# Kernel optimization log

Measured on AMD Instinct MI355X. Metric: run time of the kernel, lower is better.

The kernel has to match this reference:

```python
import jax, jax.numpy as jnp
import numpy as np

YOLO_INPUT_SIZE = 416.0
SCORE_THRESHOLD = 0.5
IOU_THRESHOLD = 0.45
AREA_THRESHOLD = 0.0005
MAX_OUTPUT_BOXES = 10
NEG = -1e9


def setup_inputs() -> dict:
    key = jax.random.key(0)
    y = jax.random.uniform(key, (64, 10647, 85), dtype=jnp.float32)
    # first 4 channels are xywh in input-pixel units (YOLO decode divides by 416)
    y = y.at[..., 0:2].multiply(YOLO_INPUT_SIZE)          # centers in [0, 416)
    y = y.at[..., 2:4].multiply(YOLO_INPUT_SIZE * 0.3)    # w,h up to ~125 px
    return {"y_pred": y}


def _decode(y_pred):
    flat = y_pred.reshape(-1, y_pred.shape[-1])           # [N, 85]
    box, conf, probs = flat[:, :4], flat[:, 4], flat[:, 5:]
    scores = conf * jnp.max(probs, axis=-1)               # [N]
    classes = jnp.argmax(probs, axis=-1).astype(jnp.int32)
    b = jnp.clip(box / YOLO_INPUT_SIZE, 0.0, 1.0)
    x, y, w, h = b[:, 0], b[:, 1], b[:, 2], b[:, 3]
    x1 = jnp.clip(x - w * 0.5, 0.0, 1.0)
    y1 = jnp.clip(y - h * 0.5, 0.0, 1.0)
    x2 = jnp.clip(x + w * 0.5, 0.0, 1.0)
    y2 = jnp.clip(y + h * 0.5, 0.0, 1.0)
    big_enough = (x2 - x1) * (y2 - y1) > AREA_THRESHOLD
    keep = big_enough & (scores > SCORE_THRESHOLD)
    boxes = jnp.stack([x1, y1, x2, y2], axis=-1)          # [N, 4]
    work = jnp.where(keep, scores, NEG)                   # masked working scores
    return boxes, scores, classes, work


def _iou_one_vs_all(ref, boxes):
    ix1 = jnp.maximum(ref[0], boxes[:, 0])
    iy1 = jnp.maximum(ref[1], boxes[:, 1])
    ix2 = jnp.minimum(ref[2], boxes[:, 2])
    iy2 = jnp.minimum(ref[3], boxes[:, 3])
    inter = jnp.maximum(ix2 - ix1, 0.0) * jnp.maximum(iy2 - iy1, 0.0)
    a_ref = (ref[2] - ref[0]) * (ref[3] - ref[1])
    a_all = (boxes[:, 2] - boxes[:, 0]) * (boxes[:, 3] - boxes[:, 1])
    return inter / (a_ref + a_all - inter + 1e-10)


def _greedy_nms(boxes, work):
    def step(w, _):
        j = jnp.argmax(w)
        v = w[j] > SCORE_THRESHOLD
        iou = _iou_one_vs_all(boxes[j], boxes)
        w = jnp.where(v & (iou > IOU_THRESHOLD), NEG, w)
        w = w.at[j].set(NEG)
        return w, (j.astype(jnp.int32), v)
    _, (idxs, valid) = jax.lax.scan(step, work, None, length=MAX_OUTPUT_BOXES)
    return idxs, valid


def reference(y_pred):
    boxes, scores, classes, work = _decode(y_pred)
    idxs, valid = _greedy_nms(boxes, work)
    # fixed-size (padded) outputs instead of dynamic boolean gather; `valid`
    # marks real detections (original returns only the valid rows)
    sel_boxes = boxes[idxs]                # [10, 4]
    sel_scores = scores[idxs][:, None]     # [10, 1]
    sel_classes = classes[idxs][:, None]   # [10, 1]
    return sel_boxes, sel_scores, sel_classes, valid
```

## Files before the change

kernel.cpp:

```cpp
#include <hip/hip_runtime.h>

#define ROWS   681408
#define NBINS  8192
#define CAP    64
#define TOPK   192
#define SELCAP 256

#define WS_ROW0     4
#define WS_CNT      16
#define WS_BUCKET   8448

__device__ __forceinline__ float clip01(float v) {
    return fminf(fmaxf(v, 0.0f), 1.0f);
}

__global__ void init_kernel(unsigned int* __restrict__ ws) {
    int i = blockIdx.x * 256 + threadIdx.x;
    if (i < NBINS) ws[WS_CNT + i] = 0u;
}

__global__ __launch_bounds__(256) void decode_kernel(
    const float* __restrict__ y, unsigned int* __restrict__ ws)
{
    const int row = blockIdx.x * 256 + threadIdx.x;
    if (row >= ROWS) return;

    const float*  p  = y + (size_t)row * 85;
    const float4* p4 = (const float4*)p;

    float4 f0 = p4[0];
    float4 f1 = p4[1];
    const float cf = f1.x;

    float bv = f1.y; int bc = 0;
    if (f1.z > bv) { bv = f1.z; bc = 1; }
    if (f1.w > bv) { bv = f1.w; bc = 2; }
    #pragma unroll
    for (int j = 2; j <= 20; j++) {
        float4 f = p4[j];
        const int b0 = 4 * j - 5;
        if (f.x > bv) { bv = f.x; bc = b0; }
        if (f.y > bv) { bv = f.y; bc = b0 + 1; }
        if (f.z > bv) { bv = f.z; bc = b0 + 2; }
        if (f.w > bv) { bv = f.w; bc = b0 + 3; }
    }
    {
        float e84 = p[84];
        if (e84 > bv) { bv = e84; bc = 79; }
    }

    const float score = cf * bv;
    float x  = clip01(f0.x / 416.0f);
    float yy = clip01(f0.y / 416.0f);
    float w  = clip01(f0.z / 416.0f);
    float h  = clip01(f0.w / 416.0f);
    float x1 = clip01(x  - w * 0.5f);
    float y1 = clip01(yy - h * 0.5f);
    float x2 = clip01(x  + w * 0.5f);
    float y2 = clip01(yy + h * 0.5f);
    bool keep = (((x2 - x1) * (y2 - y1)) > 0.0005f) && (score > 0.5f);
    if (keep) {
        int bin = (int)((score - 0.5f) * (2.0f * (float)NBINS));
        bin = min(max(bin, 0), NBINS - 1);
        unsigned int pos = atomicAdd(&ws[WS_CNT + bin], 1u);
        if (pos < (unsigned int)CAP) {
            uint2* bucket = (uint2*)&ws[WS_BUCKET];
            bucket[bin * CAP + pos] =
                make_uint2(__float_as_uint(score), (unsigned int)row);
        }
    }
    if (row == 0) {
        float* r0 = (float*)&ws[WS_ROW0];
        r0[0] = score; r0[1] = (float)bc;
        r0[2] = x1; r0[3] = y1; r0[4] = x2; r0[5] = y2;
    }
}

__global__ __launch_bounds__(256) void nms_kernel(
    const float* __restrict__ y, unsigned int* __restrict__ ws,
    float* __restrict__ out)
{
    __shared__ unsigned int chunk[256];
    __shared__ unsigned int fine[32];
    __shared__ unsigned long long keys[SELCAP];
    __shared__ float4 sboxes[SELCAP];
    __shared__ int s_coarse;
    __shared__ int s_bstar;
    __shared__ unsigned int s_m;
    __shared__ int s_picks;
    __shared__ unsigned int s_idx[10];
    __shared__ float s_score[10];
    __shared__ float4 s_box[10];
    __shared__ int s_cls[10];

    const int t = threadIdx.x;
    const uint2* bucket = (const uint2*)&ws[WS_BUCKET];

    unsigned int ssum = 0;
    {
        const uint4* cnt4 = (const uint4*)&ws[WS_CNT];
        #pragma unroll
        for (int i = 0; i < 8; i++) {
            uint4 v = cnt4[t * 8 + i];
            ssum += min(v.x, (unsigned int)CAP) + min(v.y, (unsigned int)CAP)
                  + min(v.z, (unsigned int)CAP) + min(v.w, (unsigned int)CAP);
        }
    }
    chunk[t] = ssum;
    for (int i = t; i < SELCAP; i += 256) keys[i] = 0ull;
    if (t == 0) s_m = 0u;
    __syncthreads();

    for (int off = 1; off < 256; off <<= 1) {
        unsigned int v = chunk[t];
        unsigned int a = (t + off < 256) ? chunk[t + off] : 0u;
        __syncthreads();
        chunk[t] = v + a;
        __syncthreads();
    }
    const unsigned int total  = chunk[0];
    const unsigned int target = (total < (unsigned int)TOPK) ? total
                                                             : (unsigned int)TOPK;

    if (target > 0) {
        if (chunk[t] >= target && (t == 255 || chunk[t + 1] < target))
            s_coarse = t;
        __syncthreads();

        const int cb = s_coarse * 32;
        if (t < 32) fine[t] = min(ws[WS_CNT + cb + t], (unsigned int)CAP);
        __syncthreads();
        for (int off = 1; off < 32; off <<= 1) {
            unsigned int v = 0, a = 0;
            if (t < 32) { v = fine[t]; a = (t + off < 32) ? fine[t + off] : 0u; }
            __syncthreads();
            if (t < 32) fine[t] = v + a;
            __syncthreads();
        }
        const unsigned int base = (s_coarse < 255) ? chunk[s_coarse + 1] : 0u;
        if (t < 32) {
            unsigned int sfx = base + fine[t];
            unsigned int nxt = (t == 31) ? base : base + fine[t + 1];
            if (sfx >= target && nxt < target) s_bstar = cb + t;
        }
    } else {
        if (t == 0) s_bstar = NBINS;
    }
    __syncthreads();

    for (int bin = s_bstar + t; bin < NBINS; bin += 256) {
        unsigned int c = ws[WS_CNT + bin];
        if (c > (unsigned int)CAP) c = CAP;
        for (unsigned int j = 0; j < c; j++) {
            uint2 cv = bucket[bin * CAP + j];
            unsigned int pos = atomicAdd(&s_m, 1u);
            if (pos < (unsigned int)SELCAP)
                keys[pos] = ((unsigned long long)cv.x << 32) |
                            (unsigned long long)(0xFFFFFFFFu - cv.y);
        }
    }
    __syncthreads();
    unsigned int M = s_m;
    if (M > (unsigned int)SELCAP) M = SELCAP;

    for (int k = 2; k <= SELCAP; k <<= 1) {
        for (int j = k >> 1; j > 0; j >>= 1) {
            for (int i = t; i < SELCAP; i += 256) {
                int ixj = i ^ j;
                if (ixj > i) {
                    unsigned long long a = keys[i], b = keys[ixj];
                    bool descSeg = ((i & k) == 0);
                    if (descSeg ? (a < b) : (a > b)) { keys[i] = b; keys[ixj] = a; }
                }
            }
            __syncthreads();
        }
    }

    for (int i = t; i < (int)M; i += 256) {
        unsigned int idx = 0xFFFFFFFFu - (unsigned int)(keys[i] & 0xFFFFFFFFull);
        const float* p = y + (size_t)idx * 85;
        float x  = clip01(p[0] / 416.0f);
        float yy = clip01(p[1] / 416.0f);
        float w  = clip01(p[2] / 416.0f);
        float h  = clip01(p[3] / 416.0f);
        sboxes[i] = make_float4(clip01(x - w * 0.5f), clip01(yy - h * 0.5f),
                                clip01(x + w * 0.5f), clip01(yy + h * 0.5f));
    }
    __syncthreads();

    if (t == 0) {
        int np = 0;
        for (int i = 0; i < (int)M && np < 10; i++) {
            float4 b = sboxes[i];
            bool ok = true;
            for (int kk = 0; kk < np; kk++) {
                float4 r = s_box[kk];
                float ix1 = fmaxf(r.x, b.x);
                float iy1 = fmaxf(r.y, b.y);
                float ix2 = fminf(r.z, b.z);
                float iy2 = fminf(r.w, b.w);
                float inter = fmaxf(ix2 - ix1, 0.0f) * fmaxf(iy2 - iy1, 0.0f);
                float aref = (r.z - r.x) * (r.w - r.y);
                float aall = (b.z - b.x) * (b.w - b.y);
                float iou = inter / (aref + aall - inter + 1e-10f);
                if (iou > 0.45f) { ok = false; break; }
            }
            if (ok) {
                s_box[np] = b;
                s_idx[np] = 0xFFFFFFFFu - (unsigned int)(keys[i] & 0xFFFFFFFFull);
                s_score[np] = __uint_as_float((unsigned int)(keys[i] >> 32));
                np++;
            }
        }
        s_picks = np;
    }
    __syncthreads();

    {
        int p = t >> 4, s = t & 15;
        float bv = -1.0f; int bc = 1 << 20;
        if (p < s_picks) {
            const float* pr = y + (size_t)s_idx[p] * 85 + 5;
            #pragma unroll
            for (int kk = 0; kk < 5; kk++) {
                float v = pr[s + 16 * kk];
                int c = s + 16 * kk;
                if (v > bv) { bv = v; bc = c; }
            }
        }
        #pragma unroll
        for (int m = 8; m >= 1; m >>= 1) {
            float ov = __shfl_xor(bv, m, 64);
            int   oc = __shfl_xor(bc, m, 64);
            if (ov > bv || (ov == bv && oc < bc)) { bv = ov; bc = oc; }
        }
        if (p < s_picks && s == 0) s_cls[p] = bc;
    }
    __syncthreads();

    if (t == 0) {
        const float* r0 = (const float*)&ws[WS_ROW0];
        float score0 = r0[0], class0 = r0[1];
        float4 box0 = make_float4(r0[2], r0[3], r0[4], r0[5]);
        for (int kk = 0; kk < 10; kk++) {
            bool v = kk < s_picks;
            float4 b = v ? s_box[kk] : box0;
            out[4 * kk + 0] = b.x;
            out[4 * kk + 1] = b.y;
            out[4 * kk + 2] = b.z;
            out[4 * kk + 3] = b.w;
            out[40 + kk] = v ? s_score[kk] : score0;
            out[50 + kk] = v ? (float)s_cls[kk] : class0;
            out[60 + kk] = v ? 1.0f : 0.0f;
        }
    }
}

extern "C" void kernel_launch(void* const* d_in, const int* in_sizes, int n_in,
                              void* d_out, int out_size, void* d_ws, size_t ws_size,
                              hipStream_t stream)
{
    const float* y = (const float*)d_in[0];
    unsigned int* ws = (unsigned int*)d_ws;

    init_kernel<<<dim3(NBINS / 256), dim3(256), 0, stream>>>(ws);
    decode_kernel<<<dim3((ROWS + 255) / 256), dim3(256), 0, stream>>>(y, ws);
    nms_kernel<<<dim3(1), dim3(256), 0, stream>>>(y, ws, (float*)d_out);
}
```

Baseline: 85.07 us.

## Split each row across four lanes with coalesced nontemporal loads and shuffle-reduce argmax

```diff
diff --git a/kernel.cpp b/kernel.cpp
--- a/kernel.cpp
+++ b/kernel.cpp
@@ -5,74 +5,180 @@
 #define CAP    64
 #define TOPK   192
 #define SELCAP 256
+#define RPB    128
+#define NBLK   ((ROWS + RPB - 1) / RPB)
 
 #define WS_ROW0     4
 #define WS_CNT      16
 #define WS_BUCKET   8448
 
+typedef float floatx4 __attribute__((ext_vector_type(4)));
+
 __device__ __forceinline__ float clip01(float v) {
     return fminf(fmaxf(v, 0.0f), 1.0f);
 }
 
-__global__ void init_kernel(unsigned int* __restrict__ ws) {
-    int i = blockIdx.x * 256 + threadIdx.x;
-    if (i < NBINS) ws[WS_CNT + i] = 0u;
+__device__ __forceinline__ float4 ntload4(const float4* p) {
+    floatx4 v = __builtin_nontemporal_load((const floatx4*)p);
+    return make_float4(v.x, v.y, v.z, v.w);
 }
 
 __global__ __launch_bounds__(256) void decode_kernel(
     const float* __restrict__ y, unsigned int* __restrict__ ws)
 {
-    const int row = blockIdx.x * 256 + threadIdx.x;
-    if (row >= ROWS) return;
-
-    const float*  p  = y + (size_t)row * 85;
-    const float4* p4 = (const float4*)p;
-
-    float4 f0 = p4[0];
-    float4 f1 = p4[1];
-    const float cf = f1.x;
-
-    float bv = f1.y; int bc = 0;
-    if (f1.z > bv) { bv = f1.z; bc = 1; }
-    if (f1.w > bv) { bv = f1.w; bc = 2; }
+    const int t    = threadIdx.x;
+    const int lane = t & 63;
+    const int wv   = t >> 6;
+    const int s    = lane & 3;
+    const int qr   = lane >> 2;
+    const unsigned int r0 = blockIdx.x * RPB + wv * 32 + qr * 2;
+    if (r0 >= (unsigned int)ROWS) return;
+    const unsigned int r1 = r0 + 1;
+
+    const float*  pA = y + (size_t)r0 * 85;
+    const float*  pB = pA + 85;
+    const float4* a4 = (const float4*)pA;
+    const float4* b4 = (const float4*)pB;
+
+    float4 A0 = ntload4(a4 + s);
+    float4 A1 = ntload4(a4 + s + 4);
+    float4 A2 = ntload4(a4 + s + 8);
+    float4 A3 = ntload4(a4 + s + 12);
+    float4 A4 = ntload4(a4 + s + 16);
+    float4 B0 = ntload4(b4 + s);
+    float4 B1 = ntload4(b4 + s + 4);
+    float4 B2 = ntload4(b4 + s + 8);
+    float4 B3 = ntload4(b4 + s + 12);
+    float4 B4 = ntload4(b4 + s + 16);
+    float4 At = make_float4(-1.0f, -1.0f, -1.0f, -1.0f);
+    float4 Bt = At;
+    float a84 = -1.0f, b84 = -1.0f;
+    if (s == 0) { At = ntload4(a4 + 20); Bt = ntload4(b4 + 20); }
+    if (s == 1) { a84 = pA[84]; b84 = pB[84]; }
+
+    const int b0 = 4 * s;
+    float bvA = -1.0f; int bcA = 1 << 20;
+    {
+        if (b0 + 0 >= 5 && A0.x > bvA) { bvA = A0.x; bcA = b0 - 5; }
+        if (b0 + 1 >= 5 && A0.y > bvA) { bvA = A0.y; bcA = b0 - 4; }
+        if (b0 + 2 >= 5 && A0.z > bvA) { bvA = A0.z; bcA = b0 - 3; }
+        if (b0 + 3 >= 5 && A0.w > bvA) { bvA = A0.w; bcA = b0 - 2; }
+        if (A1.x > bvA) { bvA = A1.x; bcA = b0 + 11; }
+        if (A1.y > bvA) { bvA = A1.y; bcA = b0 + 12; }
+        if (A1.z > bvA) { bvA = A1.z; bcA = b0 + 13; }
+        if (A1.w > bvA) { bvA = A1.w; bcA = b0 + 14; }
+        if (A2.x > bvA) { bvA = A2.x; bcA = b0 + 27; }
+        if (A2.y > bvA) { bvA = A2.y; bcA = b0 + 28; }
+        if (A2.z > bvA) { bvA = A2.z; bcA = b0 + 29; }
+        if (A2.w > bvA) { bvA = A2.w; bcA = b0 + 30; }
+        if (A3.x > bvA) { bvA = A3.x; bcA = b0 + 43; }
+        if (A3.y > bvA) { bvA = A3.y; bcA = b0 + 44; }
+        if (A3.z > bvA) { bvA = A3.z; bcA = b0 + 45; }
+        if (A3.w > bvA) { bvA = A3.w; bcA = b0 + 46; }
+        if (A4.x > bvA) { bvA = A4.x; bcA = b0 + 59; }
+        if (A4.y > bvA) { bvA = A4.y; bcA = b0 + 60; }
+        if (A4.z > bvA) { bvA = A4.z; bcA = b0 + 61; }
+        if (A4.w > bvA) { bvA = A4.w; bcA = b0 + 62; }
+        if (s == 0) {
+            if (At.x > bvA) { bvA = At.x; bcA = 75; }
+            if (At.y > bvA) { bvA = At.y; bcA = 76; }
+            if (At.z > bvA) { bvA = At.z; bcA = 77; }
+            if (At.w > bvA) { bvA = At.w; bcA = 78; }
+        }
+        if (s == 1 && a84 > bvA) { bvA = a84; bcA = 79; }
+    }
+    float bvB = -1.0f; int bcB = 1 << 20;
+    {
+        if (b0 + 0 >= 5 && B0.x > bvB) { bvB = B0.x; bcB = b0 - 5; }
+        if (b0 + 1 >= 5 && B0.y > bvB) { bvB = B0.y; bcB = b0 - 4; }
+        if (b0 + 2 >= 5 && B0.z > bvB) { bvB = B0.z; bcB = b0 - 3; }
+        if (b0 + 3 >= 5 && B0.w > bvB) { bvB = B0.w; bcB = b0 - 2; }
+        if (B1.x > bvB) { bvB = B1.x; bcB = b0 + 11; }
+        if (B1.y > bvB) { bvB = B1.y; bcB = b0 + 12; }
+        if (B1.z > bvB) { bvB = B1.z; bcB = b0 + 13; }
+        if (B1.w > bvB) { bvB = B1.w; bcB = b0 + 14; }
+        if (B2.x > bvB) { bvB = B2.x; bcB = b0 + 27; }
+        if (B2.y > bvB) { bvB = B2.y; bcB = b0 + 28; }
+        if (B2.z > bvB) { bvB = B2.z; bcB = b0 + 29; }
+        if (B2.w > bvB) { bvB = B2.w; bcB = b0 + 30; }
+        if (B3.x > bvB) { bvB = B3.x; bcB = b0 + 43; }
+        if (B3.y > bvB) { bvB = B3.y; bcB = b0 + 44; }
+        if (B3.z > bvB) { bvB = B3.z; bcB = b0 + 45; }
+        if (B3.w > bvB) { bvB = B3.w; bcB = b0 + 46; }
+        if (B4.x > bvB) { bvB = B4.x; bcB = b0 + 59; }
+        if (B4.y > bvB) { bvB = B4.y; bcB = b0 + 60; }
+        if (B4.z > bvB) { bvB = B4.z; bcB = b0 + 61; }
+        if (B4.w > bvB) { bvB = B4.w; bcB = b0 + 62; }
+        if (s == 0) {
+            if (Bt.x > bvB) { bvB = Bt.x; bcB = 75; }
+            if (Bt.y > bvB) { bvB = Bt.y; bcB = 76; }
+            if (Bt.z > bvB) { bvB = Bt.z; bcB = 77; }
+            if (Bt.w > bvB) { bvB = Bt.w; bcB = 78; }
+        }
+        if (s == 1 && b84 > bvB) { bvB = b84; bcB = 79; }
+    }
+
     #pragma unroll
-    for (int j = 2; j <= 20; j++) {
-        float4 f = p4[j];
-        const int b0 = 4 * j - 5;
-        if (f.x > bv) { bv = f.x; bc = b0; }
-        if (f.y > bv) { bv = f.y; bc = b0 + 1; }
-        if (f.z > bv) { bv = f.z; bc = b0 + 2; }
-        if (f.w > bv) { bv = f.w; bc = b0 + 3; }
-    }
-    {
-        float e84 = p[84];
-        if (e84 > bv) { bv = e84; bc = 79; }
-    }
-
-    const float score = cf * bv;
-    float x  = clip01(f0.x / 416.0f);
-    float yy = clip01(f0.y / 416.0f);
-    float w  = clip01(f0.z / 416.0f);
-    float h  = clip01(f0.w / 416.0f);
-    float x1 = clip01(x  - w * 0.5f);
-    float y1 = clip01(yy - h * 0.5f);
-    float x2 = clip01(x  + w * 0.5f);
-    float y2 = clip01(yy + h * 0.5f);
-    bool keep = (((x2 - x1) * (y2 - y1)) > 0.0005f) && (score > 0.5f);
-    if (keep) {
-        int bin = (int)((score - 0.5f) * (2.0f * (float)NBINS));
-        bin = min(max(bin, 0), NBINS - 1);
-        unsigned int pos = atomicAdd(&ws[WS_CNT + bin], 1u);
-        if (pos < (unsigned int)CAP) {
-            uint2* bucket = (uint2*)&ws[WS_BUCKET];
-            bucket[bin * CAP + pos] =
-                make_uint2(__float_as_uint(score), (unsigned int)row);
-        }
-    }
-    if (row == 0) {
-        float* r0 = (float*)&ws[WS_ROW0];
-        r0[0] = score; r0[1] = (float)bc;
-        r0[2] = x1; r0[3] = y1; r0[4] = x2; r0[5] = y2;
+    for (int m = 1; m <= 2; m <<= 1) {
+        float ov = __shfl_xor(bvA, m, 64);
+        int   oc = __shfl_xor(bcA, m, 64);
+        if (ov > bvA || (ov == bvA && oc < bcA)) { bvA = ov; bcA = oc; }
+        float ow = __shfl_xor(bvB, m, 64);
+        int   od = __shfl_xor(bcB, m, 64);
+        if (ow > bvB || (ow == bvB && od < bcB)) { bvB = ow; bcB = od; }
+    }
+
+    const int ql = (lane & 60) + 1;
+    float cfA = __shfl(A0.x, ql, 64);
+    float cfB = __shfl(B0.x, ql, 64);
+
+    if (s == 0) {
+        uint2* bucket = (uint2*)&ws[WS_BUCKET];
+        {
+            float score = cfA * bvA;
+            float x  = clip01(A0.x / 416.0f);
+            float yy = clip01(A0.y / 416.0f);
+            float w  = clip01(A0.z / 416.0f);
+            float h  = clip01(A0.w / 416.0f);
+            float x1 = clip01(x  - w * 0.5f);
+            float y1 = clip01(yy - h * 0.5f);
+            float x2 = clip01(x  + w * 0.5f);
+            float y2 = clip01(yy + h * 0.5f);
+            bool keep = (((x2 - x1) * (y2 - y1)) > 0.0005f) && (score > 0.5f);
+            if (keep) {
+                int bin = (int)((score - 0.5f) * (2.0f * (float)NBINS));
+                bin = min(max(bin, 0), NBINS - 1);
+                unsigned int pos = atomicAdd(&ws[WS_CNT + bin], 1u);
+                if (pos < (unsigned int)CAP)
+                    bucket[bin * CAP + pos] =
+                        make_uint2(__float_as_uint(score), r0);
+            }
+            if (r0 == 0) {
+                float* w0 = (float*)&ws[WS_ROW0];
+                w0[0] = score; w0[1] = (float)bcA;
+                w0[2] = x1; w0[3] = y1; w0[4] = x2; w0[5] = y2;
+            }
+        }
+        {
+            float score = cfB * bvB;
+            float x  = clip01(B0.x / 416.0f);
+            float yy = clip01(B0.y / 416.0f);
+            float w  = clip01(B0.z / 416.0f);
+            float h  = clip01(B0.w / 416.0f);
+            float x1 = clip01(x  - w * 0.5f);
+            float y1 = clip01(yy - h * 0.5f);
+            float x2 = clip01(x  + w * 0.5f);
+            float y2 = clip01(yy + h * 0.5f);
+            bool keep = (((x2 - x1) * (y2 - y1)) > 0.0005f) && (score > 0.5f);
+            if (keep) {
+                int bin = (int)((score - 0.5f) * (2.0f * (float)NBINS));
+                bin = min(max(bin, 0), NBINS - 1);
+                unsigned int pos = atomicAdd(&ws[WS_CNT + bin], 1u);
+                if (pos < (unsigned int)CAP)
+                    bucket[bin * CAP + pos] =
+                        make_uint2(__float_as_uint(score), r1);
+            }
+        }
     }
 }
 
@@ -264,7 +370,7 @@
     const float* y = (const float*)d_in[0];
     unsigned int* ws = (unsigned int*)d_ws;
 
-    init_kernel<<<dim3(NBINS / 256), dim3(256), 0, stream>>>(ws);
-    decode_kernel<<<dim3((ROWS + 255) / 256), dim3(256), 0, stream>>>(y, ws);
+    (void)hipMemsetAsync(d_ws, 0, (WS_CNT + NBINS) * sizeof(unsigned int), stream);
+    decode_kernel<<<dim3(NBLK), dim3(256), 0, stream>>>(y, ws);
     nms_kernel<<<dim3(1), dim3(256), 0, stream>>>(y, ws, (float*)d_out);
 }
```

Result: slower. 103.7 us (+21.9%).
